# Performance work log

Hardware: AMD Instinct MI355X
Metric: run time of the kernel (lower is better)

Reference implementation:

```python
import jax, jax.numpy as jnp
import numpy as np

V, D, H, KV, L, FF, HD = 32000, 768, 12, 4, 4, 2048, 64
N_REP = H // KV  # 3
EPS = 1e-6
ROPE_THETA = 10000.0


def setup_inputs() -> dict:
    key = jax.random.key(0)
    ks = jax.random.split(key, 12)
    s = 0.02
    return {
        'idx': jax.random.randint(ks[0], (1, 2048), 0, V),
        'embed': jax.random.normal(ks[1], (V, D), jnp.float32) * s,
        'ln1_w': jnp.ones((L, D), jnp.float32),
        'Wq': jax.random.normal(ks[2], (L, D, H * HD), jnp.float32) * s,
        'Wk': jax.random.normal(ks[3], (L, D, KV * HD), jnp.float32) * s,
        'Wv': jax.random.normal(ks[4], (L, D, KV * HD), jnp.float32) * s,
        'Wo': jax.random.normal(ks[5], (L, H * HD, D), jnp.float32) * s,
        'ln2_w': jnp.ones((L, D), jnp.float32),
        'Wg': jax.random.normal(ks[6], (L, D, FF), jnp.float32) * s,
        'Wu': jax.random.normal(ks[7], (L, D, FF), jnp.float32) * s,
        'Wd': jax.random.normal(ks[8], (L, FF, D), jnp.float32) * s,
        'normf_w': jnp.ones((D,), jnp.float32),
    }


def _rms(x, w):
    xf = x.astype(jnp.float32)
    var = jnp.mean(xf * xf, axis=-1, keepdims=True)
    return w * (xf * jax.lax.rsqrt(var + EPS)).astype(x.dtype)


def _rotate_half(x):
    x1, x2 = x[..., : x.shape[-1] // 2], x[..., x.shape[-1] // 2:]
    return jnp.concatenate((-x2, x1), axis=-1)


def reference(idx, embed, ln1_w, Wq, Wk, Wv, Wo, ln2_w, Wg, Wu, Wd, normf_w):
    B, T = idx.shape
    x = embed[idx]  # [B,T,D]

    # RoPE tables: cos/sin [1,1,T,HD]
    inv_freq = 1.0 / (ROPE_THETA ** (jnp.arange(0, HD, 2, dtype=jnp.float32) / HD))
    pos = jnp.arange(T, dtype=jnp.float32)
    freqs = pos[:, None] * inv_freq[None, :]          # [T,HD/2]
    emb = jnp.concatenate((freqs, freqs), axis=-1)     # [T,HD]
    cos = jnp.cos(emb)[None, None].astype(x.dtype)
    sin = jnp.sin(emb)[None, None].astype(x.dtype)

    causal = jnp.tril(jnp.ones((T, T), bool))[None, None]  # [1,1,T,T]
    scale = 1.0 / np.sqrt(HD)

    for l in range(L):
        # --- attention ---
        h = _rms(x, ln1_w[l])
        q = (h @ Wq[l]).reshape(B, T, H, HD).transpose(0, 2, 1, 3)   # [B,H,T,HD]
        k = (h @ Wk[l]).reshape(B, T, KV, HD).transpose(0, 2, 1, 3)  # [B,KV,T,HD]
        v = (h @ Wv[l]).reshape(B, T, KV, HD).transpose(0, 2, 1, 3)
        q = q * cos + _rotate_half(q) * sin
        k = k * cos + _rotate_half(k) * sin
        k = jnp.repeat(k, N_REP, axis=1)  # [B,H,T,HD]
        v = jnp.repeat(v, N_REP, axis=1)
        scores = jnp.einsum('bhqd,bhkd->bhqk', q, k) * scale
        scores = jnp.where(causal, scores, -jnp.inf)
        probs = jax.nn.softmax(scores.astype(jnp.float32), axis=-1).astype(q.dtype)
        attn = jnp.einsum('bhqk,bhkd->bhqd', probs, v)
        attn = attn.transpose(0, 2, 1, 3).reshape(B, T, H * HD)
        x = x + attn @ Wo[l]
        # --- gated MLP ---
        h = _rms(x, ln2_w[l])
        x = x + (jax.nn.gelu(h @ Wg[l], approximate=True) * (h @ Wu[l])) @ Wd[l]

    x = _rms(x, normf_w)
    logits = (x @ embed.T).astype(jnp.float32)  # tied lm_head
    return logits
```

## Files before the change

### kernel.cpp

```cpp
#include <hip/hip_runtime.h>

#define TSEQ 2048
#define DM   768
#define NH   12
#define NKV  4
#define HD   64
#define FFD  2048
#define NL   4
#define VOC  32000
#define QKVN 1280

typedef __attribute__((ext_vector_type(8))) short short8;
typedef __attribute__((ext_vector_type(4))) float f32x4;

__device__ __forceinline__ unsigned short f2b(float f) {
  unsigned int u = __float_as_uint(f);
  u += 0x7fffu + ((u >> 16) & 1u);
  return (unsigned short)(u >> 16);
}
__device__ __forceinline__ float b2f(unsigned short u) {
  return __uint_as_float(((unsigned int)u) << 16);
}
__device__ __forceinline__ unsigned int packbf(float a, float b) {
  return (unsigned int)f2b(a) | ((unsigned int)f2b(b) << 16);
}

__device__ __forceinline__ void gl16(const unsigned short* g, unsigned short* l) {
  __builtin_amdgcn_global_load_lds(
      (const __attribute__((address_space(1))) void*)g,
      (__attribute__((address_space(3))) void*)l, 16, 0, 0);
}

__global__ void mega_prep_kernel(const float* __restrict__ embed, unsigned short* __restrict__ embed_bf,
                                 float2* __restrict__ rope_tab,
                                 const int* __restrict__ idx, float* __restrict__ xf,
                                 const float* __restrict__ Wq, const float* __restrict__ Wk,
                                 const float* __restrict__ Wv, const float* __restrict__ Wo,
                                 const float* __restrict__ Wg, const float* __restrict__ Wu,
                                 const float* __restrict__ Wd, unsigned short* __restrict__ wts,
                                 size_t LW) {
  int blk = blockIdx.x;
  int t = threadIdx.x;
  if (blk < 24000) {
    int i = blk * 256 + t;
    float4 v = ((const float4*)embed)[i];
    uint2 o; o.x = packbf(v.x, v.y); o.y = packbf(v.z, v.w);
    ((uint2*)embed_bf)[i] = o;
    return;
  }
  if (blk < 24256) {
    int i = (blk - 24000) * 256 + t;
    int pos = i >> 5, d = i & 31;
    float inv = exp2f(-(float)d * (13.287712379549449f / 32.0f));
    float sv, cv; sincosf((float)pos * inv, &sv, &cv);
    rope_tab[i] = make_float2(cv, sv);
    return;
  }
  if (blk < 26304) {
    int row = blk - 24256;
    if (t < 192) {
      int id = idx[row];
      ((float4*)(xf + (size_t)row * DM))[t] = ((const float4*)(embed + (size_t)id * DM))[t];
    }
    return;
  }
  __shared__ float tile[32][33];
  int r = blk - 26304;
  int l = r / 6144; r -= l * 6144;
  const float* src; size_t sstr, doff; int K, N, nx;
  if (r < 576)       { src = Wq; sstr = 589824;  doff = 0;                          K = 768;  N = 768;  nx = 24; }
  else if (r < 768)  { src = Wk; sstr = 196608;  doff = 768ull * 768;               K = 768;  N = 256;  nx = 8;  r -= 576; }
  else if (r < 960)  { src = Wv; sstr = 196608;  doff = 1024ull * 768;              K = 768;  N = 256;  nx = 8;  r -= 768; }
  else if (r < 1536) { src = Wo; sstr = 589824;  doff = (size_t)QKVN * DM;          K = 768;  N = 768;  nx = 24; r -= 960; }
  else if (r < 3072) { src = Wg; sstr = 1572864; doff = (size_t)QKVN * DM + (size_t)DM * DM;
                       K = 768;  N = 2048; nx = 64; r -= 1536; }
  else if (r < 4608) { src = Wu; sstr = 1572864; doff = (size_t)QKVN * DM + (size_t)DM * DM + (size_t)FFD * DM;
                       K = 768;  N = 2048; nx = 64; r -= 3072; }
  else               { src = Wd; sstr = 1572864; doff = (size_t)QKVN * DM + (size_t)DM * DM + 2ull * FFD * DM;
                       K = 2048; N = 768;  nx = 24; r -= 4608; }
  int bx = r % nx, by = r / nx;
  src += (size_t)l * sstr;
  unsigned short* dst = wts + (size_t)l * LW + doff;
  int n0 = bx * 32, k0 = by * 32;
  int tx = t & 31, ty = t >> 5;
  #pragma unroll
  for (int i = 0; i < 4; ++i) {
    int rr = ty + i * 8;
    tile[rr][tx] = src[(size_t)(k0 + rr) * N + n0 + tx];
  }
  __syncthreads();
  #pragma unroll
  for (int i = 0; i < 4; ++i) {
    int rr = ty + i * 8;
    dst[(size_t)(n0 + rr) * K + k0 + tx] = f2b(tile[tx][rr]);
  }
}

__global__ void rmsnorm_kernel(const float* __restrict__ x,
                               const float* __restrict__ w,
                               unsigned short* __restrict__ out) {
  int row = blockIdx.x; int t = threadIdx.x;
  const float* xr = x + (size_t)row * DM;
  float v0 = xr[t], v1 = xr[t + 256], v2 = xr[t + 512];
  float s = v0*v0 + v1*v1 + v2*v2;
  #pragma unroll
  for (int off = 1; off < 64; off <<= 1) s += __shfl_xor(s, off);
  __shared__ float red[4];
  if ((t & 63) == 0) red[t >> 6] = s;
  __syncthreads();
  float tot = red[0] + red[1] + red[2] + red[3];
  float rs = rsqrtf(tot * (1.0f / DM) + 1e-6f);
  unsigned short* orow = out + (size_t)row * DM;
  orow[t]       = f2b(w[t]       * v0 * rs);
  orow[t + 256] = f2b(w[t + 256] * v1 * rs);
  orow[t + 512] = f2b(w[t + 512] * v2 * rs);
}

__global__ __launch_bounds__(512, 1) void gemm_l8_kernel(
    const unsigned short* __restrict__ A, const unsigned short* __restrict__ Bt,
    float* __restrict__ C, int N, int K) {
  __shared__ unsigned short lds[2][2][256 * 64];
  const int NT = K >> 6;
  int bid = blockIdx.x, nwg = gridDim.x;
  int wgid = (bid & 7) * (nwg >> 3) + (bid >> 3);
  int m0 = (wgid & 7) * 256;
  int n0 = (wgid >> 3) * 256;
  int tid = threadIdx.x;
  int lane = tid & 63, w = tid >> 6;
  int wm = w >> 2, wn = w & 3;
  int al = lane & 15, ag = lane >> 4;
  int swz = (al & 7) << 3;

  int rA = tid >> 3;
  int cK = ((tid & 7) * 8) ^ ((rA & 7) << 3);
  const unsigned short* Ag = A + (size_t)(m0 + rA) * K + cK;
  const unsigned short* Bg = Bt + (size_t)(n0 + rA) * K + cK;

  f32x4 acc[8][4];
  #pragma unroll
  for (int i = 0; i < 8; ++i)
    #pragma unroll
    for (int n = 0; n < 4; ++n) acc[i][n] = (f32x4){0.f, 0.f, 0.f, 0.f};

  #define STAGE(kt, c) { \
    size_t ko = (size_t)(kt) * 64; \
    unsigned short* dA = &lds[(c)][0][0] + w * 512; \
    unsigned short* dB = &lds[(c)][1][0] + w * 512; \
    gl16(Ag + (size_t)0   * K + ko, dA);            \
    gl16(Ag + (size_t)64  * K + ko, dA + 4096);     \
    gl16(Ag + (size_t)128 * K + ko, dA + 8192);     \
    gl16(Ag + (size_t)192 * K + ko, dA + 12288);    \
    gl16(Bg + (size_t)0   * K + ko, dB);            \
    gl16(Bg + (size_t)64  * K + ko, dB + 4096);     \
    gl16(Bg + (size_t)128 * K + ko, dB + 8192);     \
    gl16(Bg + (size_t)192 * K + ko, dB + 12288);    \
  }

  STAGE(0, 0);
  STAGE(1, 1);
  asm volatile("s_waitcnt vmcnt(8)" ::: "memory");
  __builtin_amdgcn_s_barrier();

  for (int t = 0; t < NT; ++t) {
    int cur = t & 1;
    const unsigned short* La = &lds[cur][0][0];
    const unsigned short* Lb = &lds[cur][1][0];
    short8 a0[8], b0[4], a1[8], b1[4];
    #pragma unroll
    for (int i = 0; i < 4; ++i)
      a0[i] = *(const short8*)&La[(wm*128 + i*16 + al)*64 + ((ag*8) ^ swz)];
    #pragma unroll
    for (int n = 0; n < 4; ++n)
      b0[n] = *(const short8*)&Lb[(wn*64 + n*16 + al)*64 + ((ag*8) ^ swz)];
    #pragma unroll
    for (int i = 4; i < 8; ++i)
      a0[i] = *(const short8*)&La[(wm*128 + i*16 + al)*64 + ((ag*8) ^ swz)];
    asm volatile("s_waitcnt lgkmcnt(4)" ::: "memory");
    __builtin_amdgcn_sched_barrier(0);
    #pragma unroll
    for (int i = 0; i < 4; ++i)
      #pragma unroll
      for (int n = 0; n < 4; ++n)
        acc[i][n] = __builtin_amdgcn_mfma_f32_16x16x32_bf16(a0[i], b0[n], acc[i][n], 0, 0, 0);
    #pragma unroll
    for (int n = 0; n < 4; ++n)
      b1[n] = *(const short8*)&Lb[(wn*64 + n*16 + al)*64 + ((32 + ag*8) ^ swz)];
    #pragma unroll
    for (int i = 0; i < 4; ++i)
      a1[i] = *(const short8*)&La[(wm*128 + i*16 + al)*64 + ((32 + ag*8) ^ swz)];
    asm volatile("s_waitcnt lgkmcnt(8)" ::: "memory");
    __builtin_amdgcn_sched_barrier(0);
    #pragma unroll
    for (int i = 4; i < 8; ++i)
      #pragma unroll
      for (int n = 0; n < 4; ++n)
        acc[i][n] = __builtin_amdgcn_mfma_f32_16x16x32_bf16(a0[i], b0[n], acc[i][n], 0, 0, 0);
    #pragma unroll
    for (int i = 4; i < 8; ++i)
      a1[i] = *(const short8*)&La[(wm*128 + i*16 + al)*64 + ((32 + ag*8) ^ swz)];
    asm volatile("s_waitcnt lgkmcnt(4)" ::: "memory");
    __builtin_amdgcn_sched_barrier(0);
    #pragma unroll
    for (int i = 0; i < 4; ++i)
      #pragma unroll
      for (int n = 0; n < 4; ++n)
        acc[i][n] = __builtin_amdgcn_mfma_f32_16x16x32_bf16(a1[i], b1[n], acc[i][n], 0, 0, 0);
    asm volatile("s_waitcnt lgkmcnt(0)" ::: "memory");
    __builtin_amdgcn_sched_barrier(0);
    __builtin_amdgcn_s_barrier();
    if (t + 2 < NT) STAGE(t + 2, cur);
    __builtin_amdgcn_s_setprio(1);
    #pragma unroll
    for (int i = 4; i < 8; ++i)
      #pragma unroll
      for (int n = 0; n < 4; ++n)
        acc[i][n] = __builtin_amdgcn_mfma_f32_16x16x32_bf16(a1[i], b1[n], acc[i][n], 0, 0, 0);
    __builtin_amdgcn_s_setprio(0);
    if (t + 2 < NT) { asm volatile("s_waitcnt vmcnt(8)" ::: "memory"); }
    else            { asm volatile("s_waitcnt vmcnt(0)" ::: "memory"); }
    __builtin_amdgcn_s_barrier();
  }
  #undef STAGE

  #pragma unroll
  for (int i = 0; i < 8; ++i)
    #pragma unroll
    for (int r = 0; r < 4; ++r) {
      float* Cr = C + (size_t)(m0 + wm*128 + i*16 + ag*4 + r) * N + n0 + wn*64 + al;
      #pragma unroll
      for (int n = 0; n < 4; ++n) Cr[n * 16] = acc[i][n][r];
    }
}

__global__ __launch_bounds__(512) void gemm_p8_kernel(
    const unsigned short* __restrict__ A, const unsigned short* __restrict__ Bt,
    float* __restrict__ C, int N, int K, int Kc) {
  __shared__ unsigned short lds[2][2][128 * 64];
  const int NT = Kc >> 6;
  int bid = blockIdx.x, nwg = gridDim.x;
  int wgid = (bid & 7) * (nwg >> 3) + (bid >> 3);
  int m0 = (wgid & 15) * 128;
  int n0 = (wgid >> 4) * 128;
  int tid = threadIdx.x;
  int lane = tid & 63, w = tid >> 6;
  int wm = w >> 2, wn = w & 3;
  int al = lane & 15, ag = lane >> 4;
  int swz = (al & 7) << 3;

  size_t koff = (size_t)blockIdx.y * Kc;
  int rp = 8 * w + (lane >> 3);
  int cK = ((lane & 7) * 8) ^ ((lane >> 3) << 3);
  const unsigned short* Ag = A + (size_t)(m0 + rp) * K + koff + cK;
  const unsigned short* Bg = Bt + (size_t)(n0 + rp) * K + koff + cK;

  f32x4 acc[4][2];
  #pragma unroll
  for (int i = 0; i < 4; ++i)
    #pragma unroll
    for (int n = 0; n < 2; ++n) acc[i][n] = (f32x4){0.f, 0.f, 0.f, 0.f};

  #define STAGE(kt, c) { \
    size_t ko = (size_t)(kt) * 64; \
    unsigned short* dA = &lds[(c)][0][0] + w * 512; \
    unsigned short* dB = &lds[(c)][1][0] + w * 512; \
    gl16(Ag + ko,                 dA);        \
    gl16(Ag + (size_t)64*K + ko,  dA + 4096); \
    gl16(Bg + ko,                 dB);        \
    gl16(Bg + (size_t)64*K + ko,  dB + 4096); \
  }

  STAGE(0, 0);
  STAGE(1, 1);
  asm volatile("s_waitcnt vmcnt(4)" ::: "memory");
  __builtin_amdgcn_s_barrier();

  for (int t = 0; t < NT; ++t) {
    int cur = t & 1;
    const unsigned short* La = &lds[cur][0][0];
    const unsigned short* Lb = &lds[cur][1][0];
    short8 a0[4], b0[2], a1[4], b1[2];
    #pragma unroll
    for (int i = 0; i < 4; ++i)
      a0[i] = *(const short8*)&La[(wm*64 + i*16 + al)*64 + ((ag*8) ^ swz)];
    #pragma unroll
    for (int n = 0; n < 2; ++n)
      b0[n] = *(const short8*)&Lb[(wn*32 + n*16 + al)*64 + ((ag*8) ^ swz)];
    #pragma unroll
    for (int i = 0; i < 4; ++i)
      a1[i] = *(const short8*)&La[(wm*64 + i*16 + al)*64 + ((32 + ag*8) ^ swz)];
    #pragma unroll
    for (int n = 0; n < 2; ++n)
      b1[n] = *(const short8*)&Lb[(wn*32 + n*16 + al)*64 + ((32 + ag*8) ^ swz)];
    asm volatile("s_waitcnt lgkmcnt(6)" ::: "memory");
    __builtin_amdgcn_sched_barrier(0);
    #pragma unroll
    for (int i = 0; i < 4; ++i)
      #pragma unroll
      for (int n = 0; n < 2; ++n)
        acc[i][n] = __builtin_amdgcn_mfma_f32_16x16x32_bf16(a0[i], b0[n], acc[i][n], 0, 0, 0);
    asm volatile("s_waitcnt lgkmcnt(0)" ::: "memory");
    __builtin_amdgcn_sched_barrier(0);
    __builtin_amdgcn_s_barrier();
    if (t + 2 < NT) STAGE(t + 2, cur);
    __builtin_amdgcn_s_setprio(1);
    #pragma unroll
    for (int i = 0; i < 4; ++i)
      #pragma unroll
      for (int n = 0; n < 2; ++n)
        acc[i][n] = __builtin_amdgcn_mfma_f32_16x16x32_bf16(a1[i], b1[n], acc[i][n], 0, 0, 0);
    __builtin_amdgcn_s_setprio(0);
    if (t + 2 < NT) { asm volatile("s_waitcnt vmcnt(4)" ::: "memory"); }
    else            { asm volatile("s_waitcnt vmcnt(0)" ::: "memory"); }
    __builtin_amdgcn_s_barrier();
  }
  #undef STAGE

  #pragma unroll
  for (int i = 0; i < 4; ++i)
    #pragma unroll
    for (int r = 0; r < 4; ++r) {
      float* Cr = C + (size_t)(m0 + wm*64 + i*16 + ag*4 + r) * N + n0 + wn*32 + al;
      #pragma unroll
      for (int n = 0; n < 2; ++n) atomicAdd(&Cr[n * 16], acc[i][n][r]);
    }
}

__device__ __forceinline__ float gelu_t(float x) {
  float x3 = x * x * x;
  return 0.5f * x * (1.0f + tanhf(0.7978845608028654f * (x + 0.044715f * x3)));
}

__global__ __launch_bounds__(512) void gemm_gu8_kernel(
    const unsigned short* __restrict__ A, const unsigned short* __restrict__ BtG,
    const unsigned short* __restrict__ BtU, unsigned short* __restrict__ Cm) {
  __shared__ unsigned short lds[2][3][128 * 64];
  const int K = DM;
  const int NT = K >> 6;
  int bid = blockIdx.x, nwg = gridDim.x;
  int wgid = (bid & 7) * (nwg >> 3) + (bid >> 3);
  int m0 = (wgid & 15) * 128;
  int n0 = (wgid >> 4) * 128;
  int tid = threadIdx.x;
  int lane = tid & 63, w = tid >> 6;
  int wm = w >> 2, wn = w & 3;
  int al = lane & 15, ag = lane >> 4;
  int swz = (al & 7) << 3;

  int rp = 8 * w + (lane >> 3);
  int cK = ((lane & 7) * 8) ^ ((lane >> 3) << 3);
  const unsigned short* Ag = A + (size_t)(m0 + rp) * K + cK;
  const unsigned short* Gg = BtG + (size_t)(n0 + rp) * K + cK;
  const unsigned short* Ug = BtU + (size_t)(n0 + rp) * K + cK;

  f32x4 accg[4][2], accu[4][2];
  #pragma unroll
  for (int i = 0; i < 4; ++i)
    #pragma unroll
    for (int n = 0; n < 2; ++n) {
      accg[i][n] = (f32x4){0.f, 0.f, 0.f, 0.f};
      accu[i][n] = (f32x4){0.f, 0.f, 0.f, 0.f};
    }

  #define STAGE(kt, c) { \
    size_t ko = (size_t)(kt) * 64; \
    unsigned short* dA = &lds[(c)][0][0] + w * 512; \
    unsigned short* dG = &lds[(c)][1][0] + w * 512; \
    unsigned short* dU = &lds[(c)][2][0] + w * 512; \
    gl16(Ag + ko,                 dA);        \
    gl16(Ag + (size_t)64*K + ko,  dA + 4096); \
    gl16(Gg + ko,                 dG);        \
    gl16(Gg + (size_t)64*K + ko,  dG + 4096); \
    gl16(Ug + ko,                 dU);        \
    gl16(Ug + (size_t)64*K + ko,  dU + 4096); \
  }

  STAGE(0, 0);
  STAGE(1, 1);
  asm volatile("s_waitcnt vmcnt(6)" ::: "memory");
  __builtin_amdgcn_s_barrier();

  for (int t = 0; t < NT; ++t) {
    int cur = t & 1;
    const unsigned short* La = &lds[cur][0][0];
    const unsigned short* Lg = &lds[cur][1][0];
    const unsigned short* Lu = &lds[cur][2][0];
    short8 a0[4], g0[2], u0[2], a1[4], g1[2], u1[2];
    #pragma unroll
    for (int i = 0; i < 4; ++i)
      a0[i] = *(const short8*)&La[(wm*64 + i*16 + al)*64 + ((ag*8) ^ swz)];
    #pragma unroll
    for (int n = 0; n < 2; ++n) {
      g0[n] = *(const short8*)&Lg[(wn*32 + n*16 + al)*64 + ((ag*8) ^ swz)];
      u0[n] = *(const short8*)&Lu[(wn*32 + n*16 + al)*64 + ((ag*8) ^ swz)];
    }
    #pragma unroll
    for (int i = 0; i < 4; ++i)
      a1[i] = *(const short8*)&La[(wm*64 + i*16 + al)*64 + ((32 + ag*8) ^ swz)];
    #pragma unroll
    for (int n = 0; n < 2; ++n) {
      g1[n] = *(const short8*)&Lg[(wn*32 + n*16 + al)*64 + ((32 + ag*8) ^ swz)];
      u1[n] = *(const short8*)&Lu[(wn*32 + n*16 + al)*64 + ((32 + ag*8) ^ swz)];
    }
    asm volatile("s_waitcnt lgkmcnt(8)" ::: "memory");
    __builtin_amdgcn_sched_barrier(0);
    #pragma unroll
    for (int i = 0; i < 4; ++i)
      #pragma unroll
      for (int n = 0; n < 2; ++n) {
        accg[i][n] = __builtin_amdgcn_mfma_f32_16x16x32_bf16(a0[i], g0[n], accg[i][n], 0, 0, 0);
        accu[i][n] = __builtin_amdgcn_mfma_f32_16x16x32_bf16(a0[i], u0[n], accu[i][n], 0, 0, 0);
      }
    asm volatile("s_waitcnt lgkmcnt(0)" ::: "memory");
    __builtin_amdgcn_sched_barrier(0);
    __builtin_amdgcn_s_barrier();
    if (t + 2 < NT) STAGE(t + 2, cur);
    __builtin_amdgcn_s_setprio(1);
    #pragma unroll
    for (int i = 0; i < 4; ++i)
      #pragma unroll
      for (int n = 0; n < 2; ++n) {
        accg[i][n] = __builtin_amdgcn_mfma_f32_16x16x32_bf16(a1[i], g1[n], accg[i][n], 0, 0, 0);
        accu[i][n] = __builtin_amdgcn_mfma_f32_16x16x32_bf16(a1[i], u1[n], accu[i][n], 0, 0, 0);
      }
    __builtin_amdgcn_s_setprio(0);
    if (t + 2 < NT) { asm volatile("s_waitcnt vmcnt(6)" ::: "memory"); }
    else            { asm volatile("s_waitcnt vmcnt(0)" ::: "memory"); }
    __builtin_amdgcn_s_barrier();
  }
  #undef STAGE

  #pragma unroll
  for (int i = 0; i < 4; ++i)
    #pragma unroll
    for (int r = 0; r < 4; ++r) {
      unsigned short* Cr = Cm + (size_t)(m0 + wm*64 + i*16 + ag*4 + r) * FFD + n0 + wn*32 + al;
      #pragma unroll
      for (int n = 0; n < 2; ++n)
        Cr[n * 16] = f2b(gelu_t(accg[i][n][r]) * accu[i][n][r]);
    }
}

__global__ __launch_bounds__(512) void gemm_qkv8_kernel(
    const unsigned short* __restrict__ A, const unsigned short* __restrict__ Bt,
    unsigned short* __restrict__ C, unsigned short* __restrict__ vT,
    const float2* __restrict__ rope_tab) {
  __shared__ unsigned short lds[2][2][128 * 64];
  const int N = QKVN, K = DM;
  const int NT = K >> 6;
  int bid = blockIdx.x, nwg = gridDim.x;
  int wgid = (bid & 7) * (nwg >> 3) + (bid >> 3);
  int m0 = (wgid & 15) * 128;
  int n0 = (wgid >> 4) * 128;
  int tid = threadIdx.x;
  int lane = tid & 63, w = tid >> 6;
  int wm = w >> 1, wn = w & 1;
  int al = lane & 15, ag = lane >> 4;
  int swz = (al & 7) << 3;

  int rp = 8 * w + (lane >> 3);
  int cK = ((lane & 7) * 8) ^ ((lane >> 3) << 3);
  const unsigned short* Ag = A + (size_t)(m0 + rp) * K + cK;
  const unsigned short* Bg = Bt + (size_t)(n0 + rp) * K + cK;

  f32x4 acc[2][4];
  #pragma unroll
  for (int i = 0; i < 2; ++i)
    #pragma unroll
    for (int n = 0; n < 4; ++n) acc[i][n] = (f32x4){0.f, 0.f, 0.f, 0.f};

  #define STAGE(kt, c) { \
    size_t ko = (size_t)(kt) * 64; \
    unsigned short* dA = &lds[(c)][0][0] + w * 512; \
    unsigned short* dB = &lds[(c)][1][0] + w * 512; \
    gl16(Ag + ko,                 dA);        \
    gl16(Ag + (size_t)64*K + ko,  dA + 4096); \
    gl16(Bg + ko,                 dB);        \
    gl16(Bg + (size_t)64*K + ko,  dB + 4096); \
  }

  STAGE(0, 0);
  STAGE(1, 1);
  asm volatile("s_waitcnt vmcnt(4)" ::: "memory");
  __builtin_amdgcn_s_barrier();

  for (int t = 0; t < NT; ++t) {
    int cur = t & 1;
    const unsigned short* La = &lds[cur][0][0];
    const unsigned short* Lb = &lds[cur][1][0];
    short8 a0[2], b0[4], a1[2], b1[4];
    #pragma unroll
    for (int i = 0; i < 2; ++i)
      a0[i] = *(const short8*)&La[(wm*32 + i*16 + al)*64 + ((ag*8) ^ swz)];
    #pragma unroll
    for (int n = 0; n < 4; ++n)
      b0[n] = *(const short8*)&Lb[(wn*64 + n*16 + al)*64 + ((ag*8) ^ swz)];
    #pragma unroll
    for (int i = 0; i < 2; ++i)
      a1[i] = *(const short8*)&La[(wm*32 + i*16 + al)*64 + ((32 + ag*8) ^ swz)];
    #pragma unroll
    for (int n = 0; n < 4; ++n)
      b1[n] = *(const short8*)&Lb[(wn*64 + n*16 + al)*64 + ((32 + ag*8) ^ swz)];
    asm volatile("s_waitcnt lgkmcnt(6)" ::: "memory");
    __builtin_amdgcn_sched_barrier(0);
    #pragma unroll
    for (int i = 0; i < 2; ++i)
      #pragma unroll
      for (int n = 0; n < 4; ++n)
        acc[i][n] = __builtin_amdgcn_mfma_f32_16x16x32_bf16(a0[i], b0[n], acc[i][n], 0, 0, 0);
    asm volatile("s_waitcnt lgkmcnt(0)" ::: "memory");
    __builtin_amdgcn_sched_barrier(0);
    __builtin_amdgcn_s_barrier();
    if (t + 2 < NT) STAGE(t + 2, cur);
    __builtin_amdgcn_s_setprio(1);
    #pragma unroll
    for (int i = 0; i < 2; ++i)
      #pragma unroll
      for (int n = 0; n < 4; ++n)
        acc[i][n] = __builtin_amdgcn_mfma_f32_16x16x32_bf16(a1[i], b1[n], acc[i][n], 0, 0, 0);
    __builtin_amdgcn_s_setprio(0);
    if (t + 2 < NT) { asm volatile("s_waitcnt vmcnt(4)" ::: "memory"); }
    else            { asm volatile("s_waitcnt vmcnt(0)" ::: "memory"); }
    __builtin_amdgcn_s_barrier();
  }
  #undef STAGE

  bool qk = (n0 + wn * 64) < 1024;
  if (qk) {
    #pragma unroll
    for (int i = 0; i < 2; ++i)
      #pragma unroll
      for (int r = 0; r < 4; ++r) {
        int pos = m0 + wm*32 + i*16 + ag*4 + r;
        unsigned short* Cr = C + (size_t)pos * N + n0 + wn*64 + al;
        #pragma unroll
        for (int n = 0; n < 2; ++n) {
          int d = n * 16 + al;
          float2 cs = rope_tab[pos * 32 + d];
          float x1 = acc[i][n][r], x2 = acc[i][n + 2][r];
          Cr[n * 16]       = f2b(x1 * cs.x - x2 * cs.y);
          Cr[(n + 2) * 16] = f2b(x2 * cs.x + x1 * cs.y);
        }
      }
  } else {
    unsigned short* scr = &lds[0][0][0] + w * 2048;
    #pragma unroll
    for (int i = 0; i < 2; ++i)
      #pragma unroll
      for (int r = 0; r < 4; ++r) {
        int posl = i*16 + ag*4 + r;
        #pragma unroll
        for (int n = 0; n < 4; ++n)
          scr[(n*16 + al) * 32 + posl] = f2b(acc[i][n][r]);
      }
    asm volatile("s_waitcnt lgkmcnt(0)" ::: "memory");
    int hb0 = n0 + wn * 64 - 1024;
    int pos0 = m0 + wm * 32;
    #pragma unroll
    for (int j = 0; j < 4; ++j) {
      int col = (lane >> 2) + j * 16;
      int pc  = (lane & 3) * 8;
      uint4 v = *(const uint4*)&scr[col * 32 + pc];
      *(uint4*)&vT[(size_t)(hb0 + col) * TSEQ + pos0 + pc] = v;
    }
  }
}

__global__ __launch_bounds__(256) void attn_chunk_kernel(
    const unsigned short* __restrict__ qkv, const unsigned short* __restrict__ vT,
    unsigned short* __restrict__ out, float* __restrict__ pO, float* __restrict__ pML) {
  __shared__ unsigned short Ks[2][64 * 64];
  __shared__ unsigned short Vt[2][64 * 64];
  __shared__ unsigned short Ps[4][16 * 64];
  int s = blockIdx.x, h = blockIdx.y;
  int qt, ci;
  if (s < 8)       { qt = s;                ci = 0; }
  else if (s < 24) { qt = 8 + ((s-8) >> 1); ci = (s-8) & 1; }
  else if (s < 48) { qt = 16 + (s-24) / 3;  ci = (s-24) % 3; }
  else             { qt = 24 + ((s-48) >> 2); ci = (s-48) & 3; }
  int nt = qt + 1;
  int t0 = ci * 8;
  int t1 = t0 + 8; if (t1 > nt) t1 = nt;
  int cnt = (nt + 7) >> 3;
  int r0 = qt * 64;
  int kvh = h / 3;
  int t = threadIdx.x;
  int lane = t & 63, w = t >> 6;
  int l16 = lane & 15, g = lane >> 4;

  int qr = r0 + w * 16 + l16;
  const unsigned short* qrow = qkv + (size_t)qr * QKVN + h * HD;
  short8 aq0 = *(const short8*)(qrow + 8 * g);
  short8 aq1 = *(const short8*)(qrow + 32 + 8 * g);

  int sw = (lane & 7) ^ (lane >> 3);
  int rloc = w * 16 + (lane >> 3);
  const unsigned short* kgb = qkv + (size_t)rloc * QKVN + DM + kvh * HD + 8 * sw;
  const unsigned short* vgb = vT + (size_t)(kvh * 64 + rloc) * TSEQ + 8 * sw;

  #define ASTAGE(kb, c) { \
    unsigned short* kd = &Ks[(c)][0] + w * 1024; \
    unsigned short* vd = &Vt[(c)][0] + w * 1024; \
    gl16(kgb + (size_t)(kb) * QKVN,       kd);       \
    gl16(kgb + (size_t)((kb) + 8) * QKVN, kd + 512); \
    gl16(vgb + (kb),                      vd);       \
    gl16(vgb + (size_t)8 * TSEQ + (kb),   vd + 512); \
  }

  f32x4 o_acc[4];
  float mrun[4], lsum[4];
  #pragma unroll
  for (int i = 0; i < 4; ++i) { o_acc[i] = (f32x4){0.f,0.f,0.f,0.f}; mrun[i] = -1e30f; lsum[i] = 0.f; }

  ASTAGE(t0 * 64, 0);
  for (int kt = t0; kt < t1; ++kt) {
    int cur = (kt - t0) & 1;
    int kb = kt * 64;
    if (kt + 1 < t1) {
      ASTAGE((kt + 1) * 64, cur ^ 1);
      asm volatile("s_waitcnt vmcnt(4)" ::: "memory");
    } else {
      asm volatile("s_waitcnt vmcnt(0)" ::: "memory");
    }
    __builtin_amdgcn_s_barrier();

    const unsigned short* Kc = &Ks[cur][0];
    const unsigned short* Vc = &Vt[cur][0];

    f32x4 s_acc[4];
    #pragma unroll
    for (int nb = 0; nb < 4; ++nb) s_acc[nb] = (f32x4){0.f,0.f,0.f,0.f};
    #pragma unroll
    for (int nb = 0; nb < 4; ++nb) {
      int key = nb * 16 + l16;
      short8 bk0 = *(const short8*)&Kc[key * 64 + ((g       ^ (key & 7)) << 3)];
      short8 bk1 = *(const short8*)&Kc[key * 64 + (((4 + g) ^ (key & 7)) << 3)];
      s_acc[nb] = __builtin_amdgcn_mfma_f32_16x16x32_bf16(aq0, bk0, s_acc[nb], 0, 0, 0);
      s_acc[nb] = __builtin_amdgcn_mfma_f32_16x16x32_bf16(aq1, bk1, s_acc[nb], 0, 0, 0);
    }

    bool diag = (kt == qt);
    #pragma unroll
    for (int r = 0; r < 4; ++r) {
      int qg = r0 + w * 16 + g * 4 + r;
      float sv[4];
      #pragma unroll
      for (int nb = 0; nb < 4; ++nb) {
        sv[nb] = s_acc[nb][r] * 0.125f;
        if (diag && (kb + nb * 16 + l16 > qg)) sv[nb] = -1e30f;
      }
      float mx = fmaxf(fmaxf(sv[0], sv[1]), fmaxf(sv[2], sv[3]));
      mx = fmaxf(mx, __shfl_xor(mx, 1));
      mx = fmaxf(mx, __shfl_xor(mx, 2));
      mx = fmaxf(mx, __shfl_xor(mx, 4));
      mx = fmaxf(mx, __shfl_xor(mx, 8));
      if (mx > mrun[r] + 8.0f) {
        float es = __expf(mrun[r] - mx);
        lsum[r] *= es;
        #pragma unroll
        for (int db = 0; db < 4; ++db) o_acc[db][r] *= es;
        mrun[r] = mx;
      }
      float rsum = 0.f;
      #pragma unroll
      for (int nb = 0; nb < 4; ++nb) { sv[nb] = __expf(sv[nb] - mrun[r]); rsum += sv[nb]; }
      lsum[r] += rsum;
      int qloc = g * 4 + r, q7 = qloc & 7;
      #pragma unroll
      for (int nb = 0; nb < 4; ++nb) {
        int key = nb * 16 + l16;
        Ps[w][qloc * 64 + ((((key >> 3) ^ q7) << 3) + (key & 7))] = f2b(sv[nb]);
      }
    }

    #pragma unroll
    for (int kc = 0; kc < 2; ++kc) {
      short8 pa = *(const short8*)&Ps[w][l16 * 64 + (((4 * kc + g) ^ (l16 & 7)) << 3)];
      #pragma unroll
      for (int db = 0; db < 4; ++db) {
        int d = db * 16 + l16;
        short8 bv = *(const short8*)&Vc[d * 64 + (((4 * kc + g) ^ (d & 7)) << 3)];
        o_acc[db] = __builtin_amdgcn_mfma_f32_16x16x32_bf16(pa, bv, o_acc[db], 0, 0, 0);
      }
    }
    __builtin_amdgcn_s_barrier();
  }
  #undef ASTAGE

  if (cnt == 1) {
    #pragma unroll
    for (int r = 0; r < 4; ++r) {
      int qg = r0 + w * 16 + g * 4 + r;
      float sr = lsum[r];
      sr += __shfl_xor(sr, 1);
      sr += __shfl_xor(sr, 2);
      sr += __shfl_xor(sr, 4);
      sr += __shfl_xor(sr, 8);
      float inv = 1.0f / sr;
      unsigned short* orow = out + (size_t)qg * DM + h * HD + l16;
      #pragma unroll
      for (int db = 0; db < 4; ++db) orow[db * 16] = f2b(o_acc[db][r] * inv);
    }
  } else {
    size_t slotg = (size_t)h * 80 + s;
    float* po = pO + slotg * 4096;
    float* pm = pML + slotg * 128;
    #pragma unroll
    for (int r = 0; r < 4; ++r) {
      int row = w * 16 + g * 4 + r;
      float sr = lsum[r];
      sr += __shfl_xor(sr, 1);
      sr += __shfl_xor(sr, 2);
      sr += __shfl_xor(sr, 4);
      sr += __shfl_xor(sr, 8);
      #pragma unroll
      for (int db = 0; db < 4; ++db) po[row * 64 + db * 16 + l16] = o_acc[db][r];
      if (l16 == 0) { pm[row * 2] = mrun[r]; pm[row * 2 + 1] = sr; }
    }
  }
}

__global__ __launch_bounds__(256) void attn_combine_kernel(
    const float* __restrict__ pO, const float* __restrict__ pML,
    unsigned short* __restrict__ out) {
  int h = blockIdx.y;
  int qt = 8 + blockIdx.x;
  int base, cnt;
  if (qt < 16)      { base = 8 + (qt - 8) * 2;  cnt = 2; }
  else if (qt < 24) { base = 24 + (qt - 16) * 3; cnt = 3; }
  else              { base = 48 + (qt - 24) * 4; cnt = 4; }
  int t = threadIdx.x;
  int row = t >> 2, d0 = (t & 3) * 16;
  float m[4], l[4];
  float M = -1e30f;
  for (int c = 0; c < cnt; ++c) {
    const float* pm = pML + ((size_t)h * 80 + base + c) * 128 + row * 2;
    m[c] = pm[0]; l[c] = pm[1];
    M = fmaxf(M, m[c]);
  }
  float o[16];
  #pragma unroll
  for (int j = 0; j < 16; ++j) o[j] = 0.f;
  float wl = 0.f;
  for (int c = 0; c < cnt; ++c) {
    float wc = __expf(m[c] - M);
    wl += wc * l[c];
    const float4* po = (const float4*)(pO + ((size_t)h * 80 + base + c) * 4096 + row * 64 + d0);
    #pragma unroll
    for (int q = 0; q < 4; ++q) {
      float4 v = po[q];
      o[q*4+0] += wc * v.x; o[q*4+1] += wc * v.y;
      o[q*4+2] += wc * v.z; o[q*4+3] += wc * v.w;
    }
  }
  float inv = 1.0f / wl;
  unsigned short* orow = out + (size_t)(qt * 64 + row) * DM + h * HD + d0;
  uint4 s0, s1;
  s0.x = packbf(o[0]*inv,  o[1]*inv);  s0.y = packbf(o[2]*inv,  o[3]*inv);
  s0.z = packbf(o[4]*inv,  o[5]*inv);  s0.w = packbf(o[6]*inv,  o[7]*inv);
  s1.x = packbf(o[8]*inv,  o[9]*inv);  s1.y = packbf(o[10]*inv, o[11]*inv);
  s1.z = packbf(o[12]*inv, o[13]*inv); s1.w = packbf(o[14]*inv, o[15]*inv);
  ((uint4*)orow)[0] = s0; ((uint4*)orow)[1] = s1;
}

extern "C" void kernel_launch(void* const* d_in, const int* in_sizes, int n_in,
                              void* d_out, int out_size, void* d_ws, size_t ws_size,
                              hipStream_t stream) {
  const int*   idx   = (const int*)d_in[0];
  const float* embed = (const float*)d_in[1];
  const float* ln1   = (const float*)d_in[2];
  const float* Wq    = (const float*)d_in[3];
  const float* Wk    = (const float*)d_in[4];
  const float* Wv    = (const float*)d_in[5];
  const float* Wo    = (const float*)d_in[6];
  const float* ln2   = (const float*)d_in[7];
  const float* Wg    = (const float*)d_in[8];
  const float* Wu    = (const float*)d_in[9];
  const float* Wd    = (const float*)d_in[10];
  const float* normf = (const float*)d_in[11];
  float* out = (float*)d_out;
  char* ws = (char*)d_ws;
  (void)in_sizes; (void)n_in; (void)out_size; (void)ws_size;

  unsigned short* embed_bf = (unsigned short*)ws;
  size_t off = (size_t)VOC * DM * 2;
  unsigned short* wts = (unsigned short*)(ws + off);
  const size_t LW = (size_t)QKVN * DM + (size_t)DM * DM
                  + 2ull * FFD * DM + (size_t)DM * FFD;
  off += LW * 2ull * NL;
  float* xf = (float*)(ws + off);            off += (size_t)TSEQ * DM * 4;
  unsigned short* h_bf = (unsigned short*)(ws + off);    off += (size_t)TSEQ * DM * 2;
  unsigned short* qkv_bf = (unsigned short*)(ws + off);  off += (size_t)TSEQ * QKVN * 2;
  unsigned short* attn_bf = (unsigned short*)(ws + off); off += (size_t)TSEQ * DM * 2;
  float* pO = (float*)(ws + off);
  unsigned short* m_bf = (unsigned short*)(ws + off);
  off += (size_t)NH * 80 * 4096 * 4;
  float* pML = (float*)(ws + off);           off += (size_t)NH * 80 * 128 * 4;
  float2* rope_tab = (float2*)(ws + off);    off += (size_t)TSEQ * 32 * 8;
  unsigned short* vT = (unsigned short*)(ws + off);      off += (size_t)NKV * HD * TSEQ * 2;

  mega_prep_kernel<<<26304 + 6144 * NL, 256, 0, stream>>>(
      embed, embed_bf, rope_tab, idx, xf, Wq, Wk, Wv, Wo, Wg, Wu, Wd, wts, LW);

  for (int l = 0; l < NL; ++l) {
    unsigned short* base = wts + (size_t)l * LW;
    unsigned short* qkvT = base;
    unsigned short* woT  = base + (size_t)QKVN * DM;
    unsigned short* wguT = woT + (size_t)DM * DM;
    unsigned short* wdT  = wguT + 2ull * FFD * DM;

    rmsnorm_kernel<<<TSEQ, 256, 0, stream>>>(xf, ln1 + (size_t)l * DM, h_bf);
    gemm_qkv8_kernel<<<(QKVN / 128) * 16, 512, 0, stream>>>(h_bf, qkvT, qkv_bf, vT, rope_tab);
    attn_chunk_kernel<<<dim3(80, NH), 256, 0, stream>>>(qkv_bf, vT, attn_bf, pO, pML);
    attn_combine_kernel<<<dim3(24, NH), 256, 0, stream>>>(pO, pML, attn_bf);
    gemm_p8_kernel<<<dim3((DM / 128) * 16, 3), 512, 0, stream>>>(attn_bf, woT, xf, DM, DM, 256);
    rmsnorm_kernel<<<TSEQ, 256, 0, stream>>>(xf, ln2 + (size_t)l * DM, h_bf);
    gemm_gu8_kernel<<<(FFD / 128) * 16, 512, 0, stream>>>(h_bf, wguT, wguT + (size_t)FFD * DM, m_bf);
    gemm_p8_kernel<<<dim3((DM / 128) * 16, 4), 512, 0, stream>>>(m_bf, wdT, xf, DM, FFD, 512);
  }

  rmsnorm_kernel<<<TSEQ, 256, 0, stream>>>(xf, normf, h_bf);
  gemm_l8_kernel<<<(VOC / 256) * (TSEQ / 256), 512, 0, stream>>>(h_bf, embed_bf, out, VOC, DM);
}
```

Measured before the change: 695.9 us.

## Batch rmsnorm rows per block, swizzle attention grid, add MFMA priority hints

The rmsnorm kernel now handles four rows per block, reusing the weight loads and launching a quarter as many blocks. The attention chunk kernel moves to a 1D grid with an XCD-style swizzle that maps blocks to (head, chunk), and raises wave priority around its MFMA sections. gemm_p8 gets a minimum-occupancy launch bound of 4, which caps registers per thread. These small tweaks aim at launch overhead, cache locality and scheduling, but the register cap could cause spills and the extra barriers in rmsnorm add serialization.

```diff
diff --git a/kernel.cpp b/kernel.cpp
--- a/kernel.cpp
+++ b/kernel.cpp
@@ -99,21 +99,27 @@
 __global__ void rmsnorm_kernel(const float* __restrict__ x,
                                const float* __restrict__ w,
                                unsigned short* __restrict__ out) {
-  int row = blockIdx.x; int t = threadIdx.x;
-  const float* xr = x + (size_t)row * DM;
-  float v0 = xr[t], v1 = xr[t + 256], v2 = xr[t + 512];
-  float s = v0*v0 + v1*v1 + v2*v2;
-  #pragma unroll
-  for (int off = 1; off < 64; off <<= 1) s += __shfl_xor(s, off);
+  int t = threadIdx.x;
+  float w0 = w[t], w1 = w[t + 256], w2 = w[t + 512];
   __shared__ float red[4];
-  if ((t & 63) == 0) red[t >> 6] = s;
-  __syncthreads();
-  float tot = red[0] + red[1] + red[2] + red[3];
-  float rs = rsqrtf(tot * (1.0f / DM) + 1e-6f);
-  unsigned short* orow = out + (size_t)row * DM;
-  orow[t]       = f2b(w[t]       * v0 * rs);
-  orow[t + 256] = f2b(w[t + 256] * v1 * rs);
-  orow[t + 512] = f2b(w[t + 512] * v2 * rs);
+  #pragma unroll
+  for (int rr = 0; rr < 4; ++rr) {
+    int row = blockIdx.x * 4 + rr;
+    const float* xr = x + (size_t)row * DM;
+    float v0 = xr[t], v1 = xr[t + 256], v2 = xr[t + 512];
+    float s = v0*v0 + v1*v1 + v2*v2;
+    #pragma unroll
+    for (int off = 1; off < 64; off <<= 1) s += __shfl_xor(s, off);
+    if ((t & 63) == 0) red[t >> 6] = s;
+    __syncthreads();
+    float tot = red[0] + red[1] + red[2] + red[3];
+    __syncthreads();
+    float rs = rsqrtf(tot * (1.0f / DM) + 1e-6f);
+    unsigned short* orow = out + (size_t)row * DM;
+    orow[t]       = f2b(w0 * v0 * rs);
+    orow[t + 256] = f2b(w1 * v1 * rs);
+    orow[t + 512] = f2b(w2 * v2 * rs);
+  }
 }
 
 __global__ __launch_bounds__(512, 1) void gemm_l8_kernel(
@@ -232,7 +238,7 @@
     }
 }
 
-__global__ __launch_bounds__(512) void gemm_p8_kernel(
+__global__ __launch_bounds__(512, 4) void gemm_p8_kernel(
     const unsigned short* __restrict__ A, const unsigned short* __restrict__ Bt,
     float* __restrict__ C, int N, int K, int Kc) {
   __shared__ unsigned short lds[2][2][128 * 64];
@@ -571,7 +577,9 @@
   __shared__ unsigned short Ks[2][64 * 64];
   __shared__ unsigned short Vt[2][64 * 64];
   __shared__ unsigned short Ps[4][16 * 64];
-  int s = blockIdx.x, h = blockIdx.y;
+  int id = blockIdx.x;
+  int swzid = (id & 7) * 120 + (id >> 3);
+  int h = swzid / 80, s = swzid % 80;
   int qt, ci;
   if (s < 8)       { qt = s;                ci = 0; }
   else if (s < 24) { qt = 8 + ((s-8) >> 1); ci = (s-8) & 1; }
@@ -629,6 +637,7 @@
     f32x4 s_acc[4];
     #pragma unroll
     for (int nb = 0; nb < 4; ++nb) s_acc[nb] = (f32x4){0.f,0.f,0.f,0.f};
+    __builtin_amdgcn_s_setprio(1);
     #pragma unroll
     for (int nb = 0; nb < 4; ++nb) {
       int key = nb * 16 + l16;
@@ -637,6 +646,7 @@
       s_acc[nb] = __builtin_amdgcn_mfma_f32_16x16x32_bf16(aq0, bk0, s_acc[nb], 0, 0, 0);
       s_acc[nb] = __builtin_amdgcn_mfma_f32_16x16x32_bf16(aq1, bk1, s_acc[nb], 0, 0, 0);
     }
+    __builtin_amdgcn_s_setprio(0);
 
     bool diag = (kt == qt);
     #pragma unroll
@@ -672,6 +682,7 @@
       }
     }
 
+    __builtin_amdgcn_s_setprio(1);
     #pragma unroll
     for (int kc = 0; kc < 2; ++kc) {
       short8 pa = *(const short8*)&Ps[w][l16 * 64 + (((4 * kc + g) ^ (l16 & 7)) << 3)];
@@ -682,6 +693,7 @@
         o_acc[db] = __builtin_amdgcn_mfma_f32_16x16x32_bf16(pa, bv, o_acc[db], 0, 0, 0);
       }
     }
+    __builtin_amdgcn_s_setprio(0);
     __builtin_amdgcn_s_barrier();
   }
   #undef ASTAGE
@@ -808,16 +820,16 @@
     unsigned short* wguT = woT + (size_t)DM * DM;
     unsigned short* wdT  = wguT + 2ull * FFD * DM;
 
-    rmsnorm_kernel<<<TSEQ, 256, 0, stream>>>(xf, ln1 + (size_t)l * DM, h_bf);
+    rmsnorm_kernel<<<TSEQ / 4, 256, 0, stream>>>(xf, ln1 + (size_t)l * DM, h_bf);
     gemm_qkv8_kernel<<<(QKVN / 128) * 16, 512, 0, stream>>>(h_bf, qkvT, qkv_bf, vT, rope_tab);
-    attn_chunk_kernel<<<dim3(80, NH), 256, 0, stream>>>(qkv_bf, vT, attn_bf, pO, pML);
+    attn_chunk_kernel<<<960, 256, 0, stream>>>(qkv_bf, vT, attn_bf, pO, pML);
     attn_combine_kernel<<<dim3(24, NH), 256, 0, stream>>>(pO, pML, attn_bf);
     gemm_p8_kernel<<<dim3((DM / 128) * 16, 3), 512, 0, stream>>>(attn_bf, woT, xf, DM, DM, 256);
-    rmsnorm_kernel<<<TSEQ, 256, 0, stream>>>(xf, ln2 + (size_t)l * DM, h_bf);
+    rmsnorm_kernel<<<TSEQ / 4, 256, 0, stream>>>(xf, ln2 + (size_t)l * DM, h_bf);
     gemm_gu8_kernel<<<(FFD / 128) * 16, 512, 0, stream>>>(h_bf, wguT, wguT + (size_t)FFD * DM, m_bf);
     gemm_p8_kernel<<<dim3((DM / 128) * 16, 4), 512, 0, stream>>>(m_bf, wdT, xf, DM, FFD, 512);
   }
 
-  rmsnorm_kernel<<<TSEQ, 256, 0, stream>>>(xf, normf, h_bf);
+  rmsnorm_kernel<<<TSEQ / 4, 256, 0, stream>>>(xf, normf, h_bf);
   gemm_l8_kernel<<<(VOC / 256) * (TSEQ / 256), 512, 0, stream>>>(h_bf, embed_bf, out, VOC, DM);
 }
```

New measurement: 710.7 us. 2.1% more time.
